# Kernel tuning notes

Hardware: AMD Instinct MI355X
Metric: run time of the kernel (lower is better)

Reference implementation:

```python
import jax, jax.numpy as jnp
import numpy as np

FREQ_NUM = 3
MAX_STEP = 4
PERIODS = np.array([24.0, 7.0, 365.0], dtype=np.float32)  # ceil(sups - infs)
INFS = np.array([0.0, 0.0, 0.0], dtype=np.float32)
BS, H, W, L, D = 128, 56, 56, 64, 128
Z_DIM = 3 * H * W + L * D + D            # 17728
EMB_DIM = 2 * FREQ_NUM                   # sin/cos per frequency
IN_DIM = Z_DIM + 2 * EMB_DIM             # 17740
HID = 4096
N_POI, N_USER = 5000, 1000


def setup_inputs() -> dict:
    key = jax.random.key(0)
    ks = jax.random.split(key, 10)
    sups = jnp.asarray(PERIODS)
    return {
        "input_freq": jax.random.uniform(ks[0], (BS, H, W), jnp.float32),
        "input_seq": jax.random.randint(ks[1], (BS, L), 0, N_POI),
        "uid": jax.random.randint(ks[2], (BS,), 0, N_USER),
        "cur_time": jax.random.uniform(ks[3], (BS, FREQ_NUM), jnp.float32) * sups,
        "tar_time": jax.random.uniform(ks[4], (BS, FREQ_NUM), jnp.float32) * sups,
        "fuse_embed": jax.random.normal(ks[5], (N_POI + N_USER, D), jnp.float32),
        "W1": jax.random.normal(ks[6], (IN_DIM, HID), jnp.float32) / np.sqrt(IN_DIM),
        "b1": jnp.zeros((HID,), jnp.float32),
        "W2": jax.random.normal(ks[7], (HID, Z_DIM), jnp.float32) / np.sqrt(HID),
        "b2": jnp.zeros((Z_DIM,), jnp.float32),
        "n_poi": N_POI,
    }


def _time_grid(cur_time, tar_time):
    # Per-sample linspace with periodic wraparound; snapshot t0_ after each
    # micro-step assignment (intended semantics of the torch loop).
    periods = jnp.asarray(PERIODS)
    frac = jnp.linspace(0.0, 1.0, MAX_STEP)  # [4]
    rows = []
    t_cur = cur_time
    for j in range(FREQ_NUM):
        s = cur_time[:, j]
        e = tar_time[:, j]
        wrap = s > e
        e_adj = jnp.where(wrap, e + periods[j], e)
        inter = s[:, None] + (e_adj - s)[:, None] * frac[None, :]  # [bs,4]
        inter = jnp.where(wrap[:, None], jnp.mod(inter, periods[j]), inter)
        for k in range(MAX_STEP):
            t_cur = t_cur.at[:, j].set(inter[:, k])
            rows.append(t_cur)
    return jnp.stack(rows, axis=0)  # [4*freq_num, bs, freq_num]


def _time_embedding(T):
    # sinusoidal embedding per frequency band
    phase = 2.0 * jnp.pi * (T - jnp.asarray(INFS)) / jnp.asarray(PERIODS)
    return jnp.concatenate([jnp.sin(phase), jnp.cos(phase)], axis=-1)  # [S,bs,2F]


def reference(input_freq, input_seq, uid, cur_time, tar_time, fuse_embed,
              W1, b1, W2, b2, n_poi):
    bs = input_freq.shape[0]
    A = jnp.tile(input_freq[:, None], (1, 3, 1, 1)).reshape(bs, -1)     # [bs,3HW]
    x = fuse_embed[input_seq].transpose(0, 2, 1).reshape(bs, -1)        # [bs,D*L]
    u = fuse_embed[n_poi + uid].reshape(bs, -1)                          # [bs,D]
    z0 = jnp.concatenate([A, x, u], axis=-1)                             # [bs,Z_DIM]

    T = _time_grid(cur_time, tar_time)
    emb = _time_embedding(T)                                             # [S,bs,2F]

    def step(z, te):
        t0e, t1e = te
        inp = jnp.concatenate([z, t0e, t1e], axis=-1)
        dz = jnp.tanh(inp @ W1 + b1) @ W2 + b2
        return z + dz, None

    z, _ = jax.lax.scan(step, z0, (emb[:-1], emb[1:]))
    return z
```

## Files before the change

### kernel.cpp

```cpp
#include <hip/hip_runtime.h>
#include <math.h>

typedef __bf16 bf16;
typedef __bf16 bf16x8 __attribute__((ext_vector_type(8)));
typedef float f32x4 __attribute__((ext_vector_type(4)));

#define ZDIM 17728
#define HIDN 4096
#define BSZ 128
#define KC1 24
#define KC2 4

__device__ __forceinline__ void gl_lds16(const bf16* g, bf16* l) {
  __builtin_amdgcn_global_load_lds(
      (const __attribute__((address_space(1))) unsigned int*)g,
      (__attribute__((address_space(3))) unsigned int*)l, 16, 0, 0);
}

__global__ void k_cast_transpose(const float* __restrict__ src, bf16* __restrict__ dst,
                                 int K, int N) {
  __shared__ float t[64][33];
  int tx = threadIdx.x, ty = threadIdx.y;
  int tid = ty * 32 + tx;
  int n0 = blockIdx.x * 32, k0 = blockIdx.y * 64;
#pragma unroll
  for (int i = 0; i < 64; i += 8)
    t[ty + i][tx] = src[(size_t)(k0 + ty + i) * N + (n0 + tx)];
  __syncthreads();
  int nl = tid >> 4;
  int kk = (tid & 15) * 4;
#pragma unroll
  for (int p = 0; p < 2; ++p) {
    int nn = nl + p * 16;
    union { bf16 h[4]; unsigned long long u; } pk;
    pk.h[0] = (bf16)t[kk + 0][nn];
    pk.h[1] = (bf16)t[kk + 1][nn];
    pk.h[2] = (bf16)t[kk + 2][nn];
    pk.h[3] = (bf16)t[kk + 3][nn];
    *(unsigned long long*)&dst[(size_t)(n0 + nn) * K + k0 + kk] = pk.u;
  }
}

__global__ void k_build_z0(const float* __restrict__ input_freq, const int* __restrict__ seq,
                           const int* __restrict__ uid, const float* __restrict__ fuse,
                           const int* __restrict__ n_poi_p,
                           float* __restrict__ z, bf16* __restrict__ zb) {
  int n = blockIdx.x * 256 + threadIdx.x;
  int b = blockIdx.y;
  if (n >= ZDIM) return;
  float v;
  if (n < 9408) {
    v = input_freq[b * 3136 + (n % 3136)];
  } else if (n < 17600) {
    int m = n - 9408;
    int d = m >> 6, l = m & 63;
    v = fuse[(size_t)seq[b * 64 + l] * 128 + d];
  } else {
    int d = n - 17600;
    v = fuse[(size_t)(n_poi_p[0] + uid[b]) * 128 + d];
  }
  size_t idx = (size_t)b * ZDIM + n;
  z[idx] = v;
  zb[idx] = (bf16)v;
}

__global__ void k_build_emb(const float* __restrict__ cur, const float* __restrict__ tar,
                            float* __restrict__ E) {
  int b = threadIdx.x;
  const float P[3] = {24.0f, 7.0f, 365.0f};
  const float TWO_PI = 6.283185307179586f;
  float t[3];
  for (int c = 0; c < 3; ++c) t[c] = cur[b * 3 + c];
  int r = 0;
  for (int j = 0; j < 3; ++j) {
    float s = cur[b * 3 + j], e = tar[b * 3 + j];
    bool wrap = s > e;
    float ea = wrap ? (e + P[j]) : e;
    for (int k = 0; k < 4; ++k) {
      float frac = (float)k / 3.0f;
      float v = s + (ea - s) * frac;
      if (wrap) v = v - floorf(v / P[j]) * P[j];
      t[j] = v;
      for (int c = 0; c < 3; ++c) {
        float ph = TWO_PI * t[c] / P[c];
        E[(r * BSZ + b) * 6 + c] = sinf(ph);
        E[(r * BSZ + b) * 6 + 3 + c] = cosf(ph);
      }
      ++r;
    }
  }
}

__global__ __launch_bounds__(256, 3) void k_gemm1(const bf16* __restrict__ A,
                                                  const bf16* __restrict__ Bt,
                                                  float* __restrict__ P) {
  __shared__ __align__(16) bf16 As[2][128 * 32];
  __shared__ __align__(16) bf16 Bs[2][128 * 32];
  const int tid = threadIdx.x;
  const int w = tid >> 6, lane = tid & 63;
  const int q = lane >> 4, r = lane & 15;
  const int nt = blockIdx.x, kc = blockIdx.y;
  const int nsteps = 23 + (kc < 2 ? 1 : 0);
  const int kstart = kc * 23 + (kc < 2 ? kc : 2);

  const int srow = lane >> 2, sslot = lane & 3;
  const int sg = sslot ^ ((srow >> 2) & 3);
  const int rA0 = (2 * w) * 16 + srow;
  const int rA1 = (2 * w + 1) * 16 + srow;
  long k0 = (long)kstart * 32;
  const bf16* pA0 = A + (size_t)rA0 * ZDIM + k0 + sg * 8;
  const bf16* pA1 = A + (size_t)rA1 * ZDIM + k0 + sg * 8;
  const bf16* pB0 = Bt + (size_t)(nt * 128 + rA0) * ZDIM + k0 + sg * 8;
  const bf16* pB1 = Bt + (size_t)(nt * 128 + rA1) * ZDIM + k0 + sg * 8;
  const int la0 = (2 * w) * 512;
  const int la1 = la0 + 512;

  const int swr = (r >> 2) & 3;
  const int aoff = r * 32 + (q ^ swr) * 8;
  const int boff0 = (32 * w + r) * 32 + (q ^ swr) * 8;
  const int boff1 = boff0 + 512;

  f32x4 zero4 = {0.f, 0.f, 0.f, 0.f};
  f32x4 acc[8][2];
#pragma unroll
  for (int mb = 0; mb < 8; ++mb) { acc[mb][0] = zero4; acc[mb][1] = zero4; }

  gl_lds16(pA0, &As[0][la0]); gl_lds16(pA1, &As[0][la1]);
  gl_lds16(pB0, &Bs[0][la0]); gl_lds16(pB1, &Bs[0][la1]);
  pA0 += 32; pA1 += 32; pB0 += 32; pB1 += 32;
  __syncthreads();

  int cur = 0;
  for (int s = 0; s < nsteps; ++s) {
    int nxt = cur ^ 1;
    if (s + 1 < nsteps) {
      gl_lds16(pA0, &As[nxt][la0]); gl_lds16(pA1, &As[nxt][la1]);
      gl_lds16(pB0, &Bs[nxt][la0]); gl_lds16(pB1, &Bs[nxt][la1]);
      pA0 += 32; pA1 += 32; pB0 += 32; pB1 += 32;
    }
    bf16x8 bfr0 = *(const bf16x8*)&Bs[cur][boff0];
    bf16x8 bfr1 = *(const bf16x8*)&Bs[cur][boff1];
#pragma unroll
    for (int mb = 0; mb < 8; ++mb) {
      bf16x8 afr = *(const bf16x8*)&As[cur][mb * 512 + aoff];
      acc[mb][0] = __builtin_amdgcn_mfma_f32_16x16x32_bf16(afr, bfr0, acc[mb][0], 0, 0, 0);
      acc[mb][1] = __builtin_amdgcn_mfma_f32_16x16x32_bf16(afr, bfr1, acc[mb][1], 0, 0, 0);
    }
    __syncthreads();
    cur = nxt;
  }

  float* Pk = P + (size_t)kc * (BSZ * HIDN);
#pragma unroll
  for (int i = 0; i < 2; ++i) {
    int n = nt * 128 + (2 * w + i) * 16 + r;
#pragma unroll
    for (int mb = 0; mb < 8; ++mb) {
#pragma unroll
      for (int reg = 0; reg < 4; ++reg) {
        int brow = mb * 16 + q * 4 + reg;
        Pk[(size_t)brow * HIDN + n] = acc[mb][i][reg];
      }
    }
  }
}

__global__ void k_epi1(const float* __restrict__ P, const float* __restrict__ b1,
                       const float* __restrict__ W1, const float* __restrict__ E,
                       int step, bf16* __restrict__ Hb) {
  int idx = blockIdx.x * 256 + threadIdx.x;
  int base = idx * 4;
  int b = base >> 12, n = base & 4095;
  f32x4 s = *(const f32x4*)&b1[n];
#pragma unroll
  for (int c = 0; c < KC1; ++c)
    s += *(const f32x4*)&P[((size_t)c * BSZ + b) * HIDN + n];
  const float* e0 = E + ((size_t)step * BSZ + b) * 6;
  const float* e1 = e0 + BSZ * 6;
#pragma unroll
  for (int j = 0; j < 6; ++j) {
    f32x4 w0 = *(const f32x4*)&W1[(size_t)(ZDIM + j) * HIDN + n];
    f32x4 w1 = *(const f32x4*)&W1[(size_t)(ZDIM + 6 + j) * HIDN + n];
    s += e0[j] * w0;
    s += e1[j] * w1;
  }
  union { bf16 h[4]; unsigned long long u; } pk;
#pragma unroll
  for (int i = 0; i < 4; ++i) pk.h[i] = (bf16)tanhf(s[i]);
  *(unsigned long long*)&Hb[base] = pk.u;
}

__global__ __launch_bounds__(256, 4) void k_gemm2(const bf16* __restrict__ A,
                                                  const bf16* __restrict__ Bt,
                                                  float* __restrict__ P2) {
  __shared__ __align__(16) bf16 As[2][128 * 32];
  __shared__ __align__(16) bf16 Bs[2][64 * 32];
  const int tid = threadIdx.x;
  const int w = tid >> 6, lane = tid & 63;
  const int q = lane >> 4, r = lane & 15;
  const int nt = blockIdx.x;
  const int kc = blockIdx.y;
  const long k0 = (long)kc * 32 * 32;

  const int srow = lane >> 2, sslot = lane & 3;
  const int sg = sslot ^ ((srow >> 2) & 3);
  const int rA0 = (2 * w) * 16 + srow;
  const int rA1 = (2 * w + 1) * 16 + srow;
  const int rB = w * 16 + srow;
  const bf16* pA0 = A + (size_t)rA0 * HIDN + k0 + sg * 8;
  const bf16* pA1 = A + (size_t)rA1 * HIDN + k0 + sg * 8;
  const bf16* pB = Bt + (size_t)(nt * 64 + rB) * HIDN + k0 + sg * 8;
  const int la0 = (2 * w) * 512;
  const int la1 = la0 + 512;
  const int lb = w * 512;

  const int swr = (r >> 2) & 3;
  const int aoff = r * 32 + (q ^ swr) * 8;
  const int boff = (w * 16 + r) * 32 + (q ^ swr) * 8;

  f32x4 zero4 = {0.f, 0.f, 0.f, 0.f};
  f32x4 acc[8];
#pragma unroll
  for (int mb = 0; mb < 8; ++mb) acc[mb] = zero4;

  gl_lds16(pA0, &As[0][la0]); gl_lds16(pA1, &As[0][la1]); gl_lds16(pB, &Bs[0][lb]);
  pA0 += 32; pA1 += 32; pB += 32;
  __syncthreads();

  int cur = 0;
  for (int s = 0; s < 32; ++s) {
    int nxt = cur ^ 1;
    if (s < 31) {
      gl_lds16(pA0, &As[nxt][la0]); gl_lds16(pA1, &As[nxt][la1]); gl_lds16(pB, &Bs[nxt][lb]);
      pA0 += 32; pA1 += 32; pB += 32;
    }
    bf16x8 bfr = *(const bf16x8*)&Bs[cur][boff];
#pragma unroll
    for (int mb = 0; mb < 8; ++mb) {
      bf16x8 afr = *(const bf16x8*)&As[cur][mb * 512 + aoff];
      acc[mb] = __builtin_amdgcn_mfma_f32_16x16x32_bf16(afr, bfr, acc[mb], 0, 0, 0);
    }
    __syncthreads();
    cur = nxt;
  }

  float* Pk = P2 + (size_t)kc * (BSZ * ZDIM);
  int n = nt * 64 + w * 16 + r;
#pragma unroll
  for (int mb = 0; mb < 8; ++mb) {
#pragma unroll
    for (int reg = 0; reg < 4; ++reg) {
      int brow = mb * 16 + q * 4 + reg;
      Pk[(size_t)brow * ZDIM + n] = acc[mb][reg];
    }
  }
}

__global__ void k_epi2(const float* __restrict__ P2, const float* __restrict__ b2,
                       float* __restrict__ z, bf16* __restrict__ zb) {
  int idx = blockIdx.x * 256 + threadIdx.x;
  size_t base = (size_t)idx * 4;
  int n = (int)(base % ZDIM);
  f32x4 s = *(const f32x4*)&b2[n];
#pragma unroll
  for (int c = 0; c < KC2; ++c)
    s += *(const f32x4*)&P2[(size_t)c * (BSZ * ZDIM) + base];
  f32x4 v = *(const f32x4*)&z[base];
  v += s;
  *(f32x4*)&z[base] = v;
  union { bf16 h[4]; unsigned long long u; } pk;
#pragma unroll
  for (int i = 0; i < 4; ++i) pk.h[i] = (bf16)v[i];
  *(unsigned long long*)&zb[base] = pk.u;
}

extern "C" void kernel_launch(void* const* d_in, const int* in_sizes, int n_in,
                              void* d_out, int out_size, void* d_ws, size_t ws_size,
                              hipStream_t stream) {
  const float* input_freq = (const float*)d_in[0];
  const int* seq = (const int*)d_in[1];
  const int* uid = (const int*)d_in[2];
  const float* cur = (const float*)d_in[3];
  const float* tar = (const float*)d_in[4];
  const float* fuse = (const float*)d_in[5];
  const float* W1 = (const float*)d_in[6];
  const float* b1 = (const float*)d_in[7];
  const float* W2 = (const float*)d_in[8];
  const float* b2 = (const float*)d_in[9];
  const int* n_poi = (const int*)d_in[10];
  float* z = (float*)d_out;

  char* ws = (char*)d_ws;
  bf16* W1t = (bf16*)ws;
  bf16* W2t = (bf16*)(ws + 145227776);
  bf16* Zb = (bf16*)(ws + 290455552);
  bf16* Hb = (bf16*)(ws + 294993920);
  float* P = (float*)(ws + 296042496);
  float* P2 = (float*)(ws + 296042496 + 50331648);
  float* E = (float*)(ws + 296042496 + 50331648 + 36306944);

  k_cast_transpose<<<dim3(HIDN / 32, ZDIM / 64), dim3(32, 8), 0, stream>>>(W1, W1t, ZDIM, HIDN);
  k_cast_transpose<<<dim3(ZDIM / 32, HIDN / 64), dim3(32, 8), 0, stream>>>(W2, W2t, HIDN, ZDIM);
  k_build_z0<<<dim3(70, BSZ), 256, 0, stream>>>(input_freq, seq, uid, fuse, n_poi, z, Zb);
  k_build_emb<<<1, BSZ, 0, stream>>>(cur, tar, E);

  for (int s = 0; s < 11; ++s) {
    k_gemm1<<<dim3(32, KC1), 256, 0, stream>>>(Zb, W1t, P);
    k_epi1<<<512, 256, 0, stream>>>(P, b1, W1, E, s, Hb);
    k_gemm2<<<dim3(277, KC2), 256, 0, stream>>>(Hb, W2t, P2);
    k_epi2<<<2216, 256, 0, stream>>>(P2, b2, z, Zb);
  }
}
```

Baseline: 2.145 ms.

## Unify GEMMs into triple-buffered kernel with 128-wide N tiles for both layers

Replaces the double-buffered GEMM main loop with a three-stage LDS ring that keeps two tile loads in flight, using explicit vmcnt waits and raw barriers instead of __syncthreads. The second GEMM now reuses the same 128x128 tile kernel, padding N to a multiple of 128 and zeroing the extra rows of the transposed W2, so partial sums are stored with a padded stride. The aim is to hide global-to-LDS latency and raise per-block MFMA reuse in the second GEMM. The cost is more LDS per block, which may lower occupancy, plus some wasted work on the padded columns.

Result: faster. 2.042 ms (-4.8%).

```diff
diff --git a/kernel.cpp b/kernel.cpp
--- a/kernel.cpp
+++ b/kernel.cpp
@@ -10,6 +10,7 @@
 #define BSZ 128
 #define KC1 24
 #define KC2 4
+#define N2PAD 17792
 
 __device__ __forceinline__ void gl_lds16(const bf16* g, bf16* l) {
   __builtin_amdgcn_global_load_lds(
@@ -39,6 +40,11 @@
     pk.h[3] = (bf16)t[kk + 3][nn];
     *(unsigned long long*)&dst[(size_t)(n0 + nn) * K + k0 + kk] = pk.u;
   }
+}
+
+__global__ void k_zero8(unsigned long long* __restrict__ p, int n8) {
+  int i = blockIdx.x * 256 + threadIdx.x;
+  if (i < n8) p[i] = 0ull;
 }
 
 __global__ void k_build_z0(const float* __restrict__ input_freq, const int* __restrict__ seq,
@@ -91,27 +97,29 @@
   }
 }
 
-__global__ __launch_bounds__(256, 3) void k_gemm1(const bf16* __restrict__ A,
-                                                  const bf16* __restrict__ Bt,
-                                                  float* __restrict__ P) {
-  __shared__ __align__(16) bf16 As[2][128 * 32];
-  __shared__ __align__(16) bf16 Bs[2][128 * 32];
+__global__ __launch_bounds__(256, 3) void k_gemm(const bf16* __restrict__ A,
+                                                 const bf16* __restrict__ Bt,
+                                                 float* __restrict__ P,
+                                                 int lda, int ldp,
+                                                 int nbase, int nextra) {
+  __shared__ __align__(16) bf16 As[3][128 * 32];
+  __shared__ __align__(16) bf16 Bs[3][128 * 32];
   const int tid = threadIdx.x;
   const int w = tid >> 6, lane = tid & 63;
   const int q = lane >> 4, r = lane & 15;
   const int nt = blockIdx.x, kc = blockIdx.y;
-  const int nsteps = 23 + (kc < 2 ? 1 : 0);
-  const int kstart = kc * 23 + (kc < 2 ? kc : 2);
+  const int nsteps = nbase + (kc < nextra ? 1 : 0);
+  const int kstart = kc * nbase + (kc < nextra ? kc : nextra);
 
   const int srow = lane >> 2, sslot = lane & 3;
   const int sg = sslot ^ ((srow >> 2) & 3);
   const int rA0 = (2 * w) * 16 + srow;
   const int rA1 = (2 * w + 1) * 16 + srow;
   long k0 = (long)kstart * 32;
-  const bf16* pA0 = A + (size_t)rA0 * ZDIM + k0 + sg * 8;
-  const bf16* pA1 = A + (size_t)rA1 * ZDIM + k0 + sg * 8;
-  const bf16* pB0 = Bt + (size_t)(nt * 128 + rA0) * ZDIM + k0 + sg * 8;
-  const bf16* pB1 = Bt + (size_t)(nt * 128 + rA1) * ZDIM + k0 + sg * 8;
+  const bf16* pA0 = A + (size_t)rA0 * lda + k0 + sg * 8;
+  const bf16* pA1 = A + (size_t)rA1 * lda + k0 + sg * 8;
+  const bf16* pB0 = Bt + (size_t)(nt * 128 + rA0) * lda + k0 + sg * 8;
+  const bf16* pB1 = Bt + (size_t)(nt * 128 + rA1) * lda + k0 + sg * 8;
   const int la0 = (2 * w) * 512;
   const int la1 = la0 + 512;
 
@@ -125,32 +133,48 @@
 #pragma unroll
   for (int mb = 0; mb < 8; ++mb) { acc[mb][0] = zero4; acc[mb][1] = zero4; }
 
-  gl_lds16(pA0, &As[0][la0]); gl_lds16(pA1, &As[0][la1]);
-  gl_lds16(pB0, &Bs[0][la0]); gl_lds16(pB1, &Bs[0][la1]);
-  pA0 += 32; pA1 += 32; pB0 += 32; pB1 += 32;
-  __syncthreads();
-
-  int cur = 0;
-  for (int s = 0; s < nsteps; ++s) {
-    int nxt = cur ^ 1;
-    if (s + 1 < nsteps) {
-      gl_lds16(pA0, &As[nxt][la0]); gl_lds16(pA1, &As[nxt][la1]);
-      gl_lds16(pB0, &Bs[nxt][la0]); gl_lds16(pB1, &Bs[nxt][la1]);
-      pA0 += 32; pA1 += 32; pB0 += 32; pB1 += 32;
-    }
-    bf16x8 bfr0 = *(const bf16x8*)&Bs[cur][boff0];
-    bf16x8 bfr1 = *(const bf16x8*)&Bs[cur][boff1];
-#pragma unroll
-    for (int mb = 0; mb < 8; ++mb) {
-      bf16x8 afr = *(const bf16x8*)&As[cur][mb * 512 + aoff];
-      acc[mb][0] = __builtin_amdgcn_mfma_f32_16x16x32_bf16(afr, bfr0, acc[mb][0], 0, 0, 0);
-      acc[mb][1] = __builtin_amdgcn_mfma_f32_16x16x32_bf16(afr, bfr1, acc[mb][1], 0, 0, 0);
-    }
-    __syncthreads();
-    cur = nxt;
-  }
-
-  float* Pk = P + (size_t)kc * (BSZ * HIDN);
+#define ISSUE(ib)                                                          \
+  {                                                                        \
+    gl_lds16(pA0, &As[ib][la0]); gl_lds16(pA1, &As[ib][la1]);              \
+    gl_lds16(pB0, &Bs[ib][la0]); gl_lds16(pB1, &Bs[ib][la1]);              \
+    pA0 += 32; pA1 += 32; pB0 += 32; pB1 += 32;                            \
+  }
+
+#define COMPUTE(ib)                                                        \
+  {                                                                        \
+    bf16x8 bfr0 = *(const bf16x8*)&Bs[ib][boff0];                          \
+    bf16x8 bfr1 = *(const bf16x8*)&Bs[ib][boff1];                          \
+    _Pragma("unroll")                                                      \
+    for (int mb = 0; mb < 8; ++mb) {                                       \
+      bf16x8 afr = *(const bf16x8*)&As[ib][mb * 512 + aoff];               \
+      acc[mb][0] = __builtin_amdgcn_mfma_f32_16x16x32_bf16(afr, bfr0, acc[mb][0], 0, 0, 0); \
+      acc[mb][1] = __builtin_amdgcn_mfma_f32_16x16x32_bf16(afr, bfr1, acc[mb][1], 0, 0, 0); \
+    }                                                                      \
+  }
+
+  ISSUE(0); ISSUE(1);
+  const int nmain = nsteps - 2;
+  for (int s = 0; s < nmain; ++s) {
+    ISSUE((s + 2) % 3);
+    asm volatile("s_waitcnt vmcnt(8)" ::: "memory");
+    __builtin_amdgcn_s_barrier();
+    COMPUTE(s % 3);
+    asm volatile("" ::: "memory");
+    __builtin_amdgcn_s_barrier();
+  }
+  asm volatile("s_waitcnt vmcnt(4)" ::: "memory");
+  __builtin_amdgcn_s_barrier();
+  COMPUTE(nmain % 3);
+  asm volatile("" ::: "memory");
+  __builtin_amdgcn_s_barrier();
+  asm volatile("s_waitcnt vmcnt(0)" ::: "memory");
+  __builtin_amdgcn_s_barrier();
+  COMPUTE((nmain + 1) % 3);
+
+#undef ISSUE
+#undef COMPUTE
+
+  float* Pk = P + (size_t)kc * (BSZ * ldp);
 #pragma unroll
   for (int i = 0; i < 2; ++i) {
     int n = nt * 128 + (2 * w + i) * 16 + r;
@@ -159,7 +183,7 @@
 #pragma unroll
       for (int reg = 0; reg < 4; ++reg) {
         int brow = mb * 16 + q * 4 + reg;
-        Pk[(size_t)brow * HIDN + n] = acc[mb][i][reg];
+        Pk[(size_t)brow * ldp + n] = acc[mb][i][reg];
       }
     }
   }
@@ -190,81 +214,17 @@
   *(unsigned long long*)&Hb[base] = pk.u;
 }
 
-__global__ __launch_bounds__(256, 4) void k_gemm2(const bf16* __restrict__ A,
-                                                  const bf16* __restrict__ Bt,
-                                                  float* __restrict__ P2) {
-  __shared__ __align__(16) bf16 As[2][128 * 32];
-  __shared__ __align__(16) bf16 Bs[2][64 * 32];
-  const int tid = threadIdx.x;
-  const int w = tid >> 6, lane = tid & 63;
-  const int q = lane >> 4, r = lane & 15;
-  const int nt = blockIdx.x;
-  const int kc = blockIdx.y;
-  const long k0 = (long)kc * 32 * 32;
-
-  const int srow = lane >> 2, sslot = lane & 3;
-  const int sg = sslot ^ ((srow >> 2) & 3);
-  const int rA0 = (2 * w) * 16 + srow;
-  const int rA1 = (2 * w + 1) * 16 + srow;
-  const int rB = w * 16 + srow;
-  const bf16* pA0 = A + (size_t)rA0 * HIDN + k0 + sg * 8;
-  const bf16* pA1 = A + (size_t)rA1 * HIDN + k0 + sg * 8;
-  const bf16* pB = Bt + (size_t)(nt * 64 + rB) * HIDN + k0 + sg * 8;
-  const int la0 = (2 * w) * 512;
-  const int la1 = la0 + 512;
-  const int lb = w * 512;
-
-  const int swr = (r >> 2) & 3;
-  const int aoff = r * 32 + (q ^ swr) * 8;
-  const int boff = (w * 16 + r) * 32 + (q ^ swr) * 8;
-
-  f32x4 zero4 = {0.f, 0.f, 0.f, 0.f};
-  f32x4 acc[8];
-#pragma unroll
-  for (int mb = 0; mb < 8; ++mb) acc[mb] = zero4;
-
-  gl_lds16(pA0, &As[0][la0]); gl_lds16(pA1, &As[0][la1]); gl_lds16(pB, &Bs[0][lb]);
-  pA0 += 32; pA1 += 32; pB += 32;
-  __syncthreads();
-
-  int cur = 0;
-  for (int s = 0; s < 32; ++s) {
-    int nxt = cur ^ 1;
-    if (s < 31) {
-      gl_lds16(pA0, &As[nxt][la0]); gl_lds16(pA1, &As[nxt][la1]); gl_lds16(pB, &Bs[nxt][lb]);
-      pA0 += 32; pA1 += 32; pB += 32;
-    }
-    bf16x8 bfr = *(const bf16x8*)&Bs[cur][boff];
-#pragma unroll
-    for (int mb = 0; mb < 8; ++mb) {
-      bf16x8 afr = *(const bf16x8*)&As[cur][mb * 512 + aoff];
-      acc[mb] = __builtin_amdgcn_mfma_f32_16x16x32_bf16(afr, bfr, acc[mb], 0, 0, 0);
-    }
-    __syncthreads();
-    cur = nxt;
-  }
-
-  float* Pk = P2 + (size_t)kc * (BSZ * ZDIM);
-  int n = nt * 64 + w * 16 + r;
-#pragma unroll
-  for (int mb = 0; mb < 8; ++mb) {
-#pragma unroll
-    for (int reg = 0; reg < 4; ++reg) {
-      int brow = mb * 16 + q * 4 + reg;
-      Pk[(size_t)brow * ZDIM + n] = acc[mb][reg];
-    }
-  }
-}
-
 __global__ void k_epi2(const float* __restrict__ P2, const float* __restrict__ b2,
                        float* __restrict__ z, bf16* __restrict__ zb) {
   int idx = blockIdx.x * 256 + threadIdx.x;
   size_t base = (size_t)idx * 4;
+  int b = (int)(base / ZDIM);
   int n = (int)(base % ZDIM);
   f32x4 s = *(const f32x4*)&b2[n];
+  size_t poff = (size_t)b * N2PAD + n;
 #pragma unroll
   for (int c = 0; c < KC2; ++c)
-    s += *(const f32x4*)&P2[(size_t)c * (BSZ * ZDIM) + base];
+    s += *(const f32x4*)&P2[(size_t)c * (BSZ * N2PAD) + poff];
   f32x4 v = *(const f32x4*)&z[base];
   v += s;
   *(f32x4*)&z[base] = v;
@@ -293,21 +253,22 @@
   char* ws = (char*)d_ws;
   bf16* W1t = (bf16*)ws;
   bf16* W2t = (bf16*)(ws + 145227776);
-  bf16* Zb = (bf16*)(ws + 290455552);
-  bf16* Hb = (bf16*)(ws + 294993920);
-  float* P = (float*)(ws + 296042496);
-  float* P2 = (float*)(ws + 296042496 + 50331648);
-  float* E = (float*)(ws + 296042496 + 50331648 + 36306944);
+  bf16* Zb = (bf16*)(ws + 290979840);
+  bf16* Hb = (bf16*)(ws + 295518208);
+  float* P = (float*)(ws + 296566784);
+  float* P2 = (float*)(ws + 346898432);
+  float* E = (float*)(ws + 383336448);
 
   k_cast_transpose<<<dim3(HIDN / 32, ZDIM / 64), dim3(32, 8), 0, stream>>>(W1, W1t, ZDIM, HIDN);
   k_cast_transpose<<<dim3(ZDIM / 32, HIDN / 64), dim3(32, 8), 0, stream>>>(W2, W2t, HIDN, ZDIM);
+  k_zero8<<<256, 256, 0, stream>>>((unsigned long long*)(W2t + (size_t)ZDIM * HIDN), 65536);
   k_build_z0<<<dim3(70, BSZ), 256, 0, stream>>>(input_freq, seq, uid, fuse, n_poi, z, Zb);
   k_build_emb<<<1, BSZ, 0, stream>>>(cur, tar, E);
 
   for (int s = 0; s < 11; ++s) {
-    k_gemm1<<<dim3(32, KC1), 256, 0, stream>>>(Zb, W1t, P);
+    k_gemm<<<dim3(32, KC1), 256, 0, stream>>>(Zb, W1t, P, ZDIM, HIDN, 23, 2);
     k_epi1<<<512, 256, 0, stream>>>(P, b1, W1, E, s, Hb);
-    k_gemm2<<<dim3(277, KC2), 256, 0, stream>>>(Hb, W2t, P2);
+    k_gemm<<<dim3(N2PAD / 128, KC2), 256, 0, stream>>>(Hb, W2t, P2, HIDN, N2PAD, 32, 0);
     k_epi2<<<2216, 256, 0, stream>>>(P2, b2, z, Zb);
   }
 }
```
